# Kernel tuning notes

Measured on AMD Instinct MI355X. Metric: run time of the kernel, lower is better.

## Reference

```python
import jax, jax.numpy as jnp
import numpy as np

N, L, S, D = 8, 1024, 4096, 512
EPS = 1e-5

def layernorm(x, g, b):
    mu = jnp.mean(x, axis=-1, keepdims=True)
    var = jnp.var(x, axis=-1, keepdims=True)
    return (x - mu) * jax.lax.rsqrt(var + EPS) * g + b

def setup_inputs() -> dict:
    key = jax.random.key(0)
    ks = jax.random.split(key, 8)
    w = lambda k, shp: jax.random.normal(k, shp, dtype=jnp.float32) * 0.02
    return {
        "x": jax.random.normal(ks[0], (N, L, D), dtype=jnp.float32),
        "source": jax.random.normal(ks[1], (N, S, D), dtype=jnp.float32),
        "Wq": w(ks[2], (D, D)),
        "Wk": w(ks[3], (D, D)),
        "Wv": w(ks[4], (D, D)),
        "Wm": w(ks[5], (D, D)),
        "W1": w(ks[6], (2 * D, 2 * D)),
        "W2": w(ks[7], (2 * D, D)),
        "g1": jnp.ones((D,), jnp.float32),
        "b1": jnp.zeros((D,), jnp.float32),
        "g2": jnp.ones((D,), jnp.float32),
        "b2": jnp.zeros((D,), jnp.float32),
    }

def reference(x, source, Wq, Wk, Wv, Wm, W1, W2, g1, b1, g2, b2):
    # projections
    q = x @ Wq          # [N, L, D]
    k = source @ Wk     # [N, S, D]
    v = source @ Wv     # [N, S, D]
    # pairwise L2 distance via ||q||^2 + ||k||^2 - 2 q.k (avoids [N,L,S,D] tensor)
    q2 = jnp.sum(q * q, axis=-1)                      # [N, L]
    k2 = jnp.sum(k * k, axis=-1)                      # [N, S]
    qk = jnp.einsum('nlc,nsc->nls', q, k)             # [N, L, S]
    dist = jnp.sqrt(jnp.maximum(q2[:, :, None] + k2[:, None, :] - 2.0 * qk, 0.0))
    attn = jax.nn.softmax(dist, axis=2)               # softmax over S (note: +distance, as in source)
    message = jnp.einsum('nls,nsc->nlc', attn, v)     # [N, L, D]
    message = layernorm(message @ Wm, g1, b1)
    h = jnp.concatenate([x, message], axis=2)         # [N, L, 2D]
    message = jax.nn.relu(h @ W1) @ W2                # [N, L, D]
    message = layernorm(message, g2, b2)
    return x + message
```

## Files before the change

kernel.cpp:

```cpp
#include <hip/hip_runtime.h>
#include <stdint.h>

typedef unsigned short u16;
typedef __attribute__((ext_vector_type(8))) short bf16x8;
typedef __attribute__((ext_vector_type(4))) float f32x4;
typedef __attribute__((ext_vector_type(4))) unsigned int u32x4;

__device__ __forceinline__ u16 f2b(float f) {
  uint32_t u = __float_as_uint(f);
  u += 0x7fffu + ((u >> 16) & 1u);
  return (u16)(u >> 16);
}
__device__ __forceinline__ float b2f(u16 h) {
  return __uint_as_float(((uint32_t)h) << 16);
}
__device__ __forceinline__ uint32_t pack2bf(float a, float b) {
#if __has_builtin(__builtin_amdgcn_cvt_pk_bf16_f32)
  typedef __attribute__((ext_vector_type(2))) __bf16 bf16x2_t;
  bf16x2_t r = __builtin_amdgcn_cvt_pk_bf16_f32(a, b);
  return __builtin_bit_cast(uint32_t, r);
#else
  return (uint32_t)f2b(a) | ((uint32_t)f2b(b) << 16);
#endif
}
__device__ __forceinline__ float fast_sqrtf(float x) {
#if __has_builtin(__builtin_amdgcn_sqrtf)
  return __builtin_amdgcn_sqrtf(x);
#else
  return sqrtf(x);
#endif
}

__device__ __forceinline__ void gload_lds16(const u16* g, u16* l) {
  __builtin_amdgcn_global_load_lds(
      (const __attribute__((address_space(1))) void*)g,
      (__attribute__((address_space(3))) void*)l, 16, 0, 0);
}

enum { EPI_BF16_T = 0, EPI_BF16_T_SQ = 1, EPI_F32_T = 2, EPI_RELU_BF16_T = 3,
       EPI_EXP_T = 4 };

template <int EPI>
__device__ __forceinline__ void gemm_body(
    u16* smem, const u16* A, size_t sA, int lda,
    const u16* B, size_t sB, int ldb,
    void* C, size_t sC, int ldc, int K, size_t pStride,
    const float* e_col2, const float* e_row2, float* e_l,
    int lin, int gx, int gy) {
  u16* As = smem;
  u16* Bs = smem + 8192;
  const int t = threadIdx.x;
  const int batch = lin & 7;
  const int rest = lin >> 3;
  const int bx = rest % gx;
  const int ry = rest / gx;
  const int by = ry % gy;
  const int part = ry / gy;
  const int m0 = by * 128, n0 = bx * 128;
  const int koff = part * K;
  const u16* Ab = A + (size_t)batch * sA + (size_t)m0 * lda + koff;
  const u16* Bb = B + (size_t)batch * sB + (size_t)n0 * ldb + koff;
  const int srow = t >> 3;
  const int skey = (srow & 3) | (((srow >> 3) & 1) << 2);
  const int scol = ((t & 7) ^ skey) << 3;
  const u16* aS = Ab + (size_t)srow * lda + scol;
  const u16* bS = Bb + (size_t)srow * ldb + scol;
  const size_t a32 = (size_t)32 * lda, b32 = (size_t)32 * ldb;
  u16* asDst = As + t * 8;
  u16* bsDst = Bs + t * 8;

  const int w = t >> 6, lane = t & 63;
  const int wm = (w >> 1) << 6, wn = (w & 1) << 6;
  const int qd = lane >> 4, l16 = lane & 15;
  const int rbase = ((l16 >> 2) << 3) + (l16 & 3);
  const int keyA = (l16 & 3) | (((l16 >> 2) & 1) << 2);
  const int keyB = (l16 & 3) | (((l16 >> 3) & 1) << 2);
  const u16* aRow0 = As + (wm + rbase) * 64;
  const u16* bRow0 = Bs + (wn + l16) * 64;

  f32x4 acc[4][4];
#pragma unroll
  for (int i = 0; i < 4; i++)
#pragma unroll
    for (int j = 0; j < 4; j++) acc[i][j] = (f32x4)0.0f;

  for (int k0 = 0; k0 < K; k0 += 64) {
    gload_lds16(aS, asDst);
    gload_lds16(aS + a32, asDst + 2048);
    gload_lds16(aS + 2 * a32, asDst + 4096);
    gload_lds16(aS + 3 * a32, asDst + 6144);
    gload_lds16(bS, bsDst);
    gload_lds16(bS + b32, bsDst + 2048);
    gload_lds16(bS + 2 * b32, bsDst + 4096);
    gload_lds16(bS + 3 * b32, bsDst + 6144);
    aS += 64;
    bS += 64;
    __syncthreads();
#pragma unroll
    for (int s = 0; s < 2; s++) {
      const int ca = (((qd | (s << 2)) ^ keyA) << 3);
      const int cb = (((qd | (s << 2)) ^ keyB) << 3);
      bf16x8 af[4], bfr[4];
      af[0] = *(const bf16x8*)(aRow0 + ca);
      af[1] = *(const bf16x8*)(aRow0 + 4 * 64 + ca);
      af[2] = *(const bf16x8*)(aRow0 + 32 * 64 + ca);
      af[3] = *(const bf16x8*)(aRow0 + 36 * 64 + ca);
#pragma unroll
      for (int i = 0; i < 4; i++)
        bfr[i] = *(const bf16x8*)(bRow0 + i * 16 * 64 + cb);
#pragma unroll
      for (int mi = 0; mi < 4; mi++)
#pragma unroll
        for (int ni = 0; ni < 4; ni++)
          acc[mi][ni] = __builtin_amdgcn_mfma_f32_16x16x32_bf16(
              af[mi], bfr[ni], acc[mi][ni], 0, 0, 0);
    }
    __syncthreads();
  }

  const size_t cbase = (size_t)part * pStride + (size_t)batch * sC;
  const int ncols = (int)(sC / ldc);

  if constexpr (EPI == EPI_EXP_T) {
    const int nrows = (int)(sA / lda);
    const float* col2 = e_col2 + (size_t)batch * ncols;
    const float* row2 = e_row2 + (size_t)batch * nrows;
    float* lb = e_l + (size_t)batch * ncols;
    float c2v[4];
#pragma unroll
    for (int ni = 0; ni < 4; ni++) c2v[ni] = col2[n0 + wn + ni * 16 + l16];
    float cs[4] = {0.f, 0.f, 0.f, 0.f};
#pragma unroll
    for (int p = 0; p < 2; p++) {
      const int prow = m0 + wm + p * 32 + qd * 8;
      float r2v[8];
#pragma unroll
      for (int r8 = 0; r8 < 8; r8++) r2v[r8] = row2[prow + r8];
#pragma unroll
      for (int ni = 0; ni < 4; ni++) {
        const int col = n0 + wn + ni * 16 + l16;
        float pv[8];
#pragma unroll
        for (int r = 0; r < 4; r++) {
          pv[r] = __expf(fast_sqrtf(
              fmaxf(c2v[ni] + r2v[r] - 2.0f * acc[2 * p][ni][r], 0.0f)));
          pv[4 + r] = __expf(fast_sqrtf(
              fmaxf(c2v[ni] + r2v[4 + r] - 2.0f * acc[2 * p + 1][ni][r], 0.0f)));
        }
#pragma unroll
        for (int j = 0; j < 8; j++) cs[ni] += pv[j];
        u32x4 wv;
        wv[0] = pack2bf(pv[0], pv[1]);
        wv[1] = pack2bf(pv[2], pv[3]);
        wv[2] = pack2bf(pv[4], pv[5]);
        wv[3] = pack2bf(pv[6], pv[7]);
        *(u32x4*)((u16*)C + cbase + (size_t)col * ldc + prow) = wv;
      }
    }
#pragma unroll
    for (int ni = 0; ni < 4; ni++) {
      cs[ni] += __shfl_xor(cs[ni], 16);
      cs[ni] += __shfl_xor(cs[ni], 32);
    }
    if (qd == 0) {
#pragma unroll
      for (int ni = 0; ni < 4; ni++)
        atomicAdd(lb + n0 + wn + ni * 16 + l16, cs[ni]);
    }
  } else if constexpr (EPI == EPI_F32_T) {
#pragma unroll
    for (int p = 0; p < 2; p++) {
      const int prow = m0 + wm + p * 32 + qd * 8;
#pragma unroll
      for (int ni = 0; ni < 4; ni++) {
        const int col = n0 + wn + ni * 16 + l16;
        float* dst = (float*)C + cbase + (size_t)col * ldc + prow;
        *(f32x4*)dst = acc[2 * p][ni];
        *(f32x4*)(dst + 4) = acc[2 * p + 1][ni];
      }
    }
  } else {
    float cs[4] = {0.f, 0.f, 0.f, 0.f};
#pragma unroll
    for (int p = 0; p < 2; p++) {
      const int prow = m0 + wm + p * 32 + qd * 8;
#pragma unroll
      for (int ni = 0; ni < 4; ni++) {
        const int col = n0 + wn + ni * 16 + l16;
        float v[8];
#pragma unroll
        for (int r = 0; r < 4; r++) {
          v[r] = acc[2 * p][ni][r];
          v[4 + r] = acc[2 * p + 1][ni][r];
        }
        if (EPI == EPI_RELU_BF16_T) {
#pragma unroll
          for (int j = 0; j < 8; j++) v[j] = fmaxf(v[j], 0.0f);
        }
        if (EPI == EPI_BF16_T_SQ) {
#pragma unroll
          for (int j = 0; j < 8; j++) cs[ni] += v[j] * v[j];
        }
        u32x4 wv;
        wv[0] = pack2bf(v[0], v[1]);
        wv[1] = pack2bf(v[2], v[3]);
        wv[2] = pack2bf(v[4], v[5]);
        wv[3] = pack2bf(v[6], v[7]);
        *(u32x4*)((u16*)C + cbase + (size_t)col * ldc + prow) = wv;
      }
    }
    if (EPI == EPI_BF16_T_SQ) {
#pragma unroll
      for (int ni = 0; ni < 4; ni++) {
        cs[ni] += __shfl_xor(cs[ni], 16);
        cs[ni] += __shfl_xor(cs[ni], 32);
      }
      if (qd == 0) {
#pragma unroll
        for (int ni = 0; ni < 4; ni++)
          atomicAdd(e_l + (size_t)batch * ncols + n0 + wn + ni * 16 + l16,
                    cs[ni]);
      }
    }
  }
}

template <int EPI>
__global__ __launch_bounds__(256, 2) void gemm_nt(
    const u16* __restrict__ A, size_t sA, int lda,
    const u16* __restrict__ B, size_t sB, int ldb,
    void* __restrict__ C, size_t sC, int ldc, int K, size_t pStride,
    const float* __restrict__ e_col2, const float* __restrict__ e_row2,
    float* __restrict__ e_l) {
  __shared__ __align__(16) u16 smem[16384];
  const int lin = blockIdx.x + gridDim.x * (blockIdx.y + gridDim.y * blockIdx.z);
  gemm_body<EPI>(smem, A, sA, lda, B, sB, ldb, C, sC, ldc, K, pStride,
                 e_col2, e_row2, e_l, lin, gridDim.x, gridDim.y);
}

__global__ __launch_bounds__(256, 2) void proj_fused(
    const u16* __restrict__ WqT, const u16* __restrict__ WkT,
    const u16* __restrict__ WvT, const u16* __restrict__ h,
    const u16* __restrict__ sb, u16* __restrict__ q, u16* __restrict__ kb,
    u16* __restrict__ vT, float* __restrict__ q2, float* __restrict__ k2) {
  __shared__ __align__(16) u16 smem[16384];
  const int lin = blockIdx.x;
  if (lin < 256) {
    gemm_body<EPI_BF16_T_SQ>(smem, WqT, 0, 512, h, (size_t)1024 * 1024, 1024,
                             q, (size_t)1024 * 512, 512, 512, 0, nullptr,
                             nullptr, q2, lin, 8, 4);
  } else if (lin < 1280) {
    gemm_body<EPI_BF16_T_SQ>(smem, WkT, 0, 512, sb, (size_t)4096 * 512, 512,
                             kb, (size_t)4096 * 512, 512, 512, 0, nullptr,
                             nullptr, k2, lin - 256, 32, 4);
  } else {
    gemm_body<EPI_BF16_T>(smem, sb, (size_t)4096 * 512, 512, WvT, 0, 512,
                          vT, (size_t)512 * 4096, 4096, 512, 0, nullptr,
                          nullptr, nullptr, lin - 1280, 4, 32);
  }
}

__global__ __launch_bounds__(256) void reduce2_div_bf16(
    const float* __restrict__ P, const float* __restrict__ l,
    u16* __restrict__ out) {
  const size_t i = (size_t)blockIdx.x * 256 + threadIdx.x;
  const float4* p = (const float4*)P;
  float4 a = p[i];
  float4 b = p[i + 1048576];
  const float inv = 1.0f / l[i >> 7];
  ushort4 o = make_ushort4(f2b((a.x + b.x) * inv), f2b((a.y + b.y) * inv),
                           f2b((a.z + b.z) * inv), f2b((a.w + b.w) * inv));
  *(ushort4*)(out + (i << 2)) = o;
}

__global__ __launch_bounds__(256) void fused_prep(
    const float* __restrict__ x, const float* __restrict__ sc,
    u16* __restrict__ h, u16* __restrict__ sb, float* __restrict__ q2,
    float* __restrict__ k2, float* __restrict__ lsum) {
  const size_t i = (size_t)blockIdx.x * 256 + threadIdx.x;
  if (i < 1048576) {
    const float4 f = ((const float4*)x)[i];
    const int e = (int)(i << 2);
    const int row = e >> 9, col = e & 511;
    *(ushort4*)(h + ((size_t)row << 10) + col) =
        make_ushort4(f2b(f.x), f2b(f.y), f2b(f.z), f2b(f.w));
  } else if (i < 5242880) {
    const size_t j = i - 1048576;
    const float4 f = ((const float4*)sc)[j];
    *(ushort4*)(sb + (j << 2)) =
        make_ushort4(f2b(f.x), f2b(f.y), f2b(f.z), f2b(f.w));
  } else {
    const size_t j = i - 5242880;
    const float4 z = {0.f, 0.f, 0.f, 0.f};
    if (j < 2048) ((float4*)q2)[j] = z;
    else if (j < 10240) ((float4*)k2)[j - 2048] = z;
    else ((float4*)lsum)[j - 10240] = z;
  }
}

__global__ void transpose_w6(
    const float* __restrict__ Wq, const float* __restrict__ Wk,
    const float* __restrict__ Wv, const float* __restrict__ Wm,
    const float* __restrict__ W1, const float* __restrict__ W2,
    u16* __restrict__ WqT, u16* __restrict__ WkT, u16* __restrict__ WvT,
    u16* __restrict__ WmT, u16* __restrict__ W1T, u16* __restrict__ W2T) {
  __shared__ float tile[32][33];
  const float* W;
  u16* WT;
  int R, Cn;
  switch (blockIdx.z) {
    case 0: W = Wq; WT = WqT; R = 512; Cn = 512; break;
    case 1: W = Wk; WT = WkT; R = 512; Cn = 512; break;
    case 2: W = Wv; WT = WvT; R = 512; Cn = 512; break;
    case 3: W = Wm; WT = WmT; R = 512; Cn = 512; break;
    case 4: W = W1; WT = W1T; R = 1024; Cn = 1024; break;
    default: W = W2; WT = W2T; R = 1024; Cn = 512; break;
  }
  const int c0 = blockIdx.x * 32, r0 = blockIdx.y * 32;
  if (c0 >= Cn || r0 >= R) return;
  const int tx = threadIdx.x, ty = threadIdx.y;
  for (int i = ty; i < 32; i += 8) tile[i][tx] = W[(size_t)(r0 + i) * Cn + c0 + tx];
  __syncthreads();
  for (int i = ty; i < 32; i += 8) WT[(size_t)(c0 + i) * R + r0 + tx] = f2b(tile[tx][i]);
}

__global__ __launch_bounds__(128) void ln_to_h(const float* __restrict__ mm,
                                               const float* __restrict__ g,
                                               const float* __restrict__ b,
                                               u16* __restrict__ h) {
  const size_t row = blockIdx.x;
  const int t = threadIdx.x;
  const float4 fa = ((const float4*)(mm + row * 512))[t];
  const float4 fb = ((const float4*)(mm + 4194304 + row * 512))[t];
  float4 f;
  f.x = fa.x + fb.x; f.y = fa.y + fb.y; f.z = fa.z + fb.z; f.w = fa.w + fb.w;
  float s = f.x + f.y + f.z + f.w;
  float sq = f.x * f.x + f.y * f.y + f.z * f.z + f.w * f.w;
#pragma unroll
  for (int off = 32; off; off >>= 1) { s += __shfl_xor(s, off); sq += __shfl_xor(sq, off); }
  __shared__ float rs_[2], rq_[2];
  if ((t & 63) == 0) { rs_[t >> 6] = s; rq_[t >> 6] = sq; }
  __syncthreads();
  s = rs_[0] + rs_[1]; sq = rq_[0] + rq_[1];
  const float mu = s * (1.0f / 512.0f);
  const float rstd = rsqrtf(sq * (1.0f / 512.0f) - mu * mu + 1e-5f);
  const float4 gv = ((const float4*)g)[t], bv = ((const float4*)b)[t];
  ushort4 o = make_ushort4(f2b((f.x - mu) * rstd * gv.x + bv.x),
                           f2b((f.y - mu) * rstd * gv.y + bv.y),
                           f2b((f.z - mu) * rstd * gv.z + bv.z),
                           f2b((f.w - mu) * rstd * gv.w + bv.w));
  *(ushort4*)(h + (row << 10) + 512 + (t << 2)) = o;
}

__global__ __launch_bounds__(128) void ln_residual(const float* __restrict__ m2,
                                                   const float* __restrict__ x,
                                                   const float* __restrict__ g,
                                                   const float* __restrict__ b,
                                                   float* __restrict__ out) {
  const size_t row = blockIdx.x;
  const int t = threadIdx.x;
  const float4 fa = ((const float4*)(m2 + row * 512))[t];
  const float4 fb = ((const float4*)(m2 + 4194304 + row * 512))[t];
  float4 f;
  f.x = fa.x + fb.x; f.y = fa.y + fb.y; f.z = fa.z + fb.z; f.w = fa.w + fb.w;
  float s = f.x + f.y + f.z + f.w;
  float sq = f.x * f.x + f.y * f.y + f.z * f.z + f.w * f.w;
#pragma unroll
  for (int off = 32; off; off >>= 1) { s += __shfl_xor(s, off); sq += __shfl_xor(sq, off); }
  __shared__ float rs_[2], rq_[2];
  if ((t & 63) == 0) { rs_[t >> 6] = s; rq_[t >> 6] = sq; }
  __syncthreads();
  s = rs_[0] + rs_[1]; sq = rq_[0] + rq_[1];
  const float mu = s * (1.0f / 512.0f);
  const float rstd = rsqrtf(sq * (1.0f / 512.0f) - mu * mu + 1e-5f);
  const float4 gv = ((const float4*)g)[t], bv = ((const float4*)b)[t];
  const float4 xv = ((const float4*)(x + row * 512))[t];
  float4 o;
  o.x = xv.x + (f.x - mu) * rstd * gv.x + bv.x;
  o.y = xv.y + (f.y - mu) * rstd * gv.y + bv.y;
  o.z = xv.z + (f.z - mu) * rstd * gv.z + bv.z;
  o.w = xv.w + (f.w - mu) * rstd * gv.w + bv.w;
  ((float4*)(out + row * 512))[t] = o;
}

extern "C" void kernel_launch(void* const* d_in, const int* in_sizes, int n_in,
                              void* d_out, int out_size, void* d_ws, size_t ws_size,
                              hipStream_t stream) {
  const float* x  = (const float*)d_in[0];
  const float* sc = (const float*)d_in[1];
  const float* Wq = (const float*)d_in[2];
  const float* Wk = (const float*)d_in[3];
  const float* Wv = (const float*)d_in[4];
  const float* Wm = (const float*)d_in[5];
  const float* W1 = (const float*)d_in[6];
  const float* W2 = (const float*)d_in[7];
  const float* g1 = (const float*)d_in[8];
  const float* b1 = (const float*)d_in[9];
  const float* g2 = (const float*)d_in[10];
  const float* b2 = (const float*)d_in[11];
  float* out = (float*)d_out;
  char* ws = (char*)d_ws;

  constexpr int N = 8, L = 1024, S = 4096, D = 512;
  u16*   h   = (u16*)(ws + 0);
  u16*   sb  = (u16*)(ws + 16777216);
  u16*   WqT = (u16*)(ws + 50331648);
  u16*   WkT = (u16*)(ws + 50855936);
  u16*   WvT = (u16*)(ws + 51380224);
  u16*   WmT = (u16*)(ws + 51904512);
  u16*   W1T = (u16*)(ws + 52428800);
  u16*   W2T = (u16*)(ws + 54525952);
  u16*   q   = (u16*)(ws + 55574528);
  u16*   kb  = (u16*)(ws + 63963136);
  u16*   vT  = (u16*)(ws + 97517568);
  float* lsum= (float*)(ws + 131072000);
  float* q2  = (float*)(ws + 164626432);
  float* k2  = (float*)(ws + 164659200);
  u16*   qk  = (u16*)(ws + 164790272);
  u16*   msg = (u16*)(ws + 55574528);
  float* mpart = (float*)(ws + 63963136);
  float* mm  = (float*)(ws + 63963136);
  u16*   hh  = (u16*)(ws + 80740352);
  float* m2  = (float*)(ws + 97517568);

  fused_prep<<<dim3(20528), 256, 0, stream>>>(x, sc, h, sb, q2, k2, lsum);
  transpose_w6<<<dim3(32, 32, 6), dim3(32, 8), 0, stream>>>(
      Wq, Wk, Wv, Wm, W1, W2, WqT, WkT, WvT, WmT, W1T, W2T);

  proj_fused<<<dim3(2304), 256, 0, stream>>>(WqT, WkT, WvT, h, sb, q, kb, vT,
                                             q2, k2);

  gemm_nt<EPI_EXP_T><<<dim3(8, 32, 8), 256, 0, stream>>>(
      kb, (size_t)S * 512, 512, q, (size_t)L * 512, 512, qk, (size_t)L * S, S,
      512, 0, q2, k2, lsum);
  gemm_nt<EPI_F32_T><<<dim3(8, 4, 16), 256, 0, stream>>>(
      vT, (size_t)D * S, S, qk, (size_t)L * S, S, mpart, (size_t)L * 512, 512,
      2048, (size_t)(N * L) * 512, nullptr, nullptr, nullptr);
  reduce2_div_bf16<<<dim3(4096), 256, 0, stream>>>(mpart, lsum, msg);

  gemm_nt<EPI_F32_T><<<dim3(8, 4, 16), 256, 0, stream>>>(
      WmT, 0, 512, msg, (size_t)L * 512, 512, mm, (size_t)L * 512, 512, 256,
      (size_t)(N * L) * 512, nullptr, nullptr, nullptr);
  ln_to_h<<<dim3(N * L), 128, 0, stream>>>(mm, g1, b1, h);

  gemm_nt<EPI_RELU_BF16_T><<<dim3(8, 8, 8), 256, 0, stream>>>(
      W1T, 0, 1024, h, (size_t)L * 1024, 1024, hh, (size_t)L * 1024, 1024, 1024,
      0, nullptr, nullptr, nullptr);
  gemm_nt<EPI_F32_T><<<dim3(8, 4, 16), 256, 0, stream>>>(
      W2T, 0, 1024, hh, (size_t)L * 1024, 1024, m2, (size_t)L * 512, 512, 512,
      (size_t)(N * L) * 512, nullptr, nullptr, nullptr);

  ln_residual<<<dim3(N * L), 128, 0, stream>>>(m2, x, g2, b2, out);
}
```

Baseline: 355.3 us.

## Merge prep kernels, fold split-K reduce into Wm GEMM via duplicated weights

Merges the input conversion and weight transpose launches into one prep kernel. The split-K attention-times-V partials are now written as bf16 side by side (row width 1024). The Wm projection consumes them against a horizontally duplicated WmT, so the K-sum happens inside that GEMM and the 1/lsum normalization moves into ln_to_h. This removes the reduce2_div kernel and its fp32 partial round-trip. It also swaps the block index order for the q/k projections. The risk is that rounding the unnormalized partials to bf16 changes precision, and the Wm GEMM now runs a K of 1024 instead of 512.

```diff
diff --git a/kernel.cpp b/kernel.cpp
--- a/kernel.cpp
+++ b/kernel.cpp
@@ -40,7 +40,7 @@
 enum { EPI_BF16_T = 0, EPI_BF16_T_SQ = 1, EPI_F32_T = 2, EPI_RELU_BF16_T = 3,
        EPI_EXP_T = 4 };
 
-template <int EPI>
+template <int EPI, bool BYFAST = false>
 __device__ __forceinline__ void gemm_body(
     u16* smem, const u16* A, size_t sA, int lda,
     const u16* B, size_t sB, int ldb,
@@ -52,10 +52,18 @@
   const int t = threadIdx.x;
   const int batch = lin & 7;
   const int rest = lin >> 3;
-  const int bx = rest % gx;
-  const int ry = rest / gx;
-  const int by = ry % gy;
-  const int part = ry / gy;
+  int bx, by, part;
+  if (BYFAST) {
+    by = rest % gy;
+    const int rx = rest / gy;
+    bx = rx % gx;
+    part = rx / gx;
+  } else {
+    bx = rest % gx;
+    const int ry = rest / gx;
+    by = ry % gy;
+    part = ry / gy;
+  }
   const int m0 = by * 128, n0 = bx * 128;
   const int koff = part * K;
   const u16* Ab = A + (size_t)batch * sA + (size_t)m0 * lda + koff;
@@ -246,13 +254,13 @@
   __shared__ __align__(16) u16 smem[16384];
   const int lin = blockIdx.x;
   if (lin < 256) {
-    gemm_body<EPI_BF16_T_SQ>(smem, WqT, 0, 512, h, (size_t)1024 * 1024, 1024,
-                             q, (size_t)1024 * 512, 512, 512, 0, nullptr,
-                             nullptr, q2, lin, 8, 4);
+    gemm_body<EPI_BF16_T_SQ, true>(smem, WqT, 0, 512, h, (size_t)1024 * 1024,
+                                   1024, q, (size_t)1024 * 512, 512, 512, 0,
+                                   nullptr, nullptr, q2, lin, 8, 4);
   } else if (lin < 1280) {
-    gemm_body<EPI_BF16_T_SQ>(smem, WkT, 0, 512, sb, (size_t)4096 * 512, 512,
-                             kb, (size_t)4096 * 512, 512, 512, 0, nullptr,
-                             nullptr, k2, lin - 256, 32, 4);
+    gemm_body<EPI_BF16_T_SQ, true>(smem, WkT, 0, 512, sb, (size_t)4096 * 512,
+                                   512, kb, (size_t)4096 * 512, 512, 512, 0,
+                                   nullptr, nullptr, k2, lin - 256, 32, 4);
   } else {
     gemm_body<EPI_BF16_T>(smem, sb, (size_t)4096 * 512, 512, WvT, 0, 512,
                           vT, (size_t)512 * 4096, 4096, 512, 0, nullptr,
@@ -260,80 +268,86 @@
   }
 }
 
-__global__ __launch_bounds__(256) void reduce2_div_bf16(
-    const float* __restrict__ P, const float* __restrict__ l,
-    u16* __restrict__ out) {
-  const size_t i = (size_t)blockIdx.x * 256 + threadIdx.x;
-  const float4* p = (const float4*)P;
-  float4 a = p[i];
-  float4 b = p[i + 1048576];
-  const float inv = 1.0f / l[i >> 7];
-  ushort4 o = make_ushort4(f2b((a.x + b.x) * inv), f2b((a.y + b.y) * inv),
-                           f2b((a.z + b.z) * inv), f2b((a.w + b.w) * inv));
-  *(ushort4*)(out + (i << 2)) = o;
-}
-
-__global__ __launch_bounds__(256) void fused_prep(
+__global__ __launch_bounds__(256) void prep_all(
     const float* __restrict__ x, const float* __restrict__ sc,
     u16* __restrict__ h, u16* __restrict__ sb, float* __restrict__ q2,
-    float* __restrict__ k2, float* __restrict__ lsum) {
-  const size_t i = (size_t)blockIdx.x * 256 + threadIdx.x;
-  if (i < 1048576) {
-    const float4 f = ((const float4*)x)[i];
-    const int e = (int)(i << 2);
-    const int row = e >> 9, col = e & 511;
-    *(ushort4*)(h + ((size_t)row << 10) + col) =
-        make_ushort4(f2b(f.x), f2b(f.y), f2b(f.z), f2b(f.w));
-  } else if (i < 5242880) {
-    const size_t j = i - 1048576;
-    const float4 f = ((const float4*)sc)[j];
-    *(ushort4*)(sb + (j << 2)) =
-        make_ushort4(f2b(f.x), f2b(f.y), f2b(f.z), f2b(f.w));
-  } else {
-    const size_t j = i - 5242880;
-    const float4 z = {0.f, 0.f, 0.f, 0.f};
-    if (j < 2048) ((float4*)q2)[j] = z;
-    else if (j < 10240) ((float4*)k2)[j - 2048] = z;
-    else ((float4*)lsum)[j - 10240] = z;
-  }
-}
-
-__global__ void transpose_w6(
+    float* __restrict__ k2, float* __restrict__ lsum,
     const float* __restrict__ Wq, const float* __restrict__ Wk,
     const float* __restrict__ Wv, const float* __restrict__ Wm,
     const float* __restrict__ W1, const float* __restrict__ W2,
     u16* __restrict__ WqT, u16* __restrict__ WkT, u16* __restrict__ WvT,
-    u16* __restrict__ WmT, u16* __restrict__ W1T, u16* __restrict__ W2T) {
+    u16* __restrict__ WmT2, u16* __restrict__ W1T, u16* __restrict__ W2T) {
   __shared__ float tile[32][33];
+  const int blk = blockIdx.x;
+  if (blk < 20528) {
+    const size_t i = (size_t)blk * 256 + threadIdx.x;
+    if (i < 1048576) {
+      const float4 f = ((const float4*)x)[i];
+      const int e = (int)(i << 2);
+      const int row = e >> 9, col = e & 511;
+      *(ushort4*)(h + ((size_t)row << 10) + col) =
+          make_ushort4(f2b(f.x), f2b(f.y), f2b(f.z), f2b(f.w));
+    } else if (i < 5242880) {
+      const size_t j = i - 1048576;
+      const float4 f = ((const float4*)sc)[j];
+      *(ushort4*)(sb + (j << 2)) =
+          make_ushort4(f2b(f.x), f2b(f.y), f2b(f.z), f2b(f.w));
+    } else {
+      const size_t j = i - 5242880;
+      const float4 z = {0.f, 0.f, 0.f, 0.f};
+      if (j < 2048) ((float4*)q2)[j] = z;
+      else if (j < 10240) ((float4*)k2)[j - 2048] = z;
+      else ((float4*)lsum)[j - 10240] = z;
+    }
+    return;
+  }
+  const int tb = blk - 20528;
   const float* W;
   u16* WT;
-  int R, Cn;
-  switch (blockIdx.z) {
-    case 0: W = Wq; WT = WqT; R = 512; Cn = 512; break;
-    case 1: W = Wk; WT = WkT; R = 512; Cn = 512; break;
-    case 2: W = Wv; WT = WvT; R = 512; Cn = 512; break;
-    case 3: W = Wm; WT = WmT; R = 512; Cn = 512; break;
-    case 4: W = W1; WT = W1T; R = 1024; Cn = 1024; break;
-    default: W = W2; WT = W2T; R = 1024; Cn = 512; break;
-  }
-  const int c0 = blockIdx.x * 32, r0 = blockIdx.y * 32;
-  if (c0 >= Cn || r0 >= R) return;
-  const int tx = threadIdx.x, ty = threadIdx.y;
-  for (int i = ty; i < 32; i += 8) tile[i][tx] = W[(size_t)(r0 + i) * Cn + c0 + tx];
+  int R, Cn, ldT, dup = 0, c0, r0;
+  if (tb < 1024) {
+    const int z = tb >> 8, local = tb & 255;
+    switch (z) {
+      case 0: W = Wq; WT = WqT; break;
+      case 1: W = Wk; WT = WkT; break;
+      case 2: W = Wv; WT = WvT; break;
+      default: W = Wm; WT = WmT2; dup = 1; break;
+    }
+    R = 512; Cn = 512; ldT = dup ? 1024 : 512;
+    c0 = (local & 15) << 5; r0 = (local >> 4) << 5;
+  } else if (tb < 2048) {
+    const int local = tb - 1024;
+    W = W1; WT = W1T; R = 1024; Cn = 1024; ldT = 1024;
+    c0 = (local & 31) << 5; r0 = (local >> 5) << 5;
+  } else {
+    const int local = tb - 2048;
+    W = W2; WT = W2T; R = 1024; Cn = 512; ldT = 1024;
+    c0 = (local & 15) << 5; r0 = (local >> 4) << 5;
+  }
+  const int tx = threadIdx.x & 31, ty = threadIdx.x >> 5;
+  for (int i = ty; i < 32; i += 8)
+    tile[i][tx] = W[(size_t)(r0 + i) * Cn + c0 + tx];
   __syncthreads();
-  for (int i = ty; i < 32; i += 8) WT[(size_t)(c0 + i) * R + r0 + tx] = f2b(tile[tx][i]);
+  for (int i = ty; i < 32; i += 8) {
+    const u16 v = f2b(tile[tx][i]);
+    WT[(size_t)(c0 + i) * ldT + r0 + tx] = v;
+    if (dup) WT[(size_t)(c0 + i) * ldT + 512 + r0 + tx] = v;
+  }
 }
 
 __global__ __launch_bounds__(128) void ln_to_h(const float* __restrict__ mm,
+                                               const float* __restrict__ lsum,
                                                const float* __restrict__ g,
                                                const float* __restrict__ b,
                                                u16* __restrict__ h) {
   const size_t row = blockIdx.x;
   const int t = threadIdx.x;
+  const float inv = 1.0f / lsum[row];
   const float4 fa = ((const float4*)(mm + row * 512))[t];
   const float4 fb = ((const float4*)(mm + 4194304 + row * 512))[t];
   float4 f;
-  f.x = fa.x + fb.x; f.y = fa.y + fb.y; f.z = fa.z + fb.z; f.w = fa.w + fb.w;
+  f.x = (fa.x + fb.x) * inv; f.y = (fa.y + fb.y) * inv;
+  f.z = (fa.z + fb.z) * inv; f.w = (fa.w + fb.w) * inv;
   float s = f.x + f.y + f.z + f.w;
   float sq = f.x * f.x + f.y * f.y + f.z * f.z + f.w * f.w;
 #pragma unroll
@@ -402,30 +416,29 @@
   char* ws = (char*)d_ws;
 
   constexpr int N = 8, L = 1024, S = 4096, D = 512;
-  u16*   h   = (u16*)(ws + 0);
-  u16*   sb  = (u16*)(ws + 16777216);
-  u16*   WqT = (u16*)(ws + 50331648);
-  u16*   WkT = (u16*)(ws + 50855936);
-  u16*   WvT = (u16*)(ws + 51380224);
-  u16*   WmT = (u16*)(ws + 51904512);
-  u16*   W1T = (u16*)(ws + 52428800);
-  u16*   W2T = (u16*)(ws + 54525952);
-  u16*   q   = (u16*)(ws + 55574528);
-  u16*   kb  = (u16*)(ws + 63963136);
-  u16*   vT  = (u16*)(ws + 97517568);
-  float* lsum= (float*)(ws + 131072000);
-  float* q2  = (float*)(ws + 164626432);
-  float* k2  = (float*)(ws + 164659200);
-  u16*   qk  = (u16*)(ws + 164790272);
-  u16*   msg = (u16*)(ws + 55574528);
-  float* mpart = (float*)(ws + 63963136);
-  float* mm  = (float*)(ws + 63963136);
-  u16*   hh  = (u16*)(ws + 80740352);
-  float* m2  = (float*)(ws + 97517568);
-
-  fused_prep<<<dim3(20528), 256, 0, stream>>>(x, sc, h, sb, q2, k2, lsum);
-  transpose_w6<<<dim3(32, 32, 6), dim3(32, 8), 0, stream>>>(
-      Wq, Wk, Wv, Wm, W1, W2, WqT, WkT, WvT, WmT, W1T, W2T);
+  u16*   h    = (u16*)(ws + 0);
+  u16*   sb   = (u16*)(ws + 16777216);
+  u16*   WqT  = (u16*)(ws + 50331648);
+  u16*   WkT  = (u16*)(ws + 50855936);
+  u16*   WvT  = (u16*)(ws + 51380224);
+  u16*   WmT2 = (u16*)(ws + 51904512);
+  u16*   W1T  = (u16*)(ws + 52953088);
+  u16*   W2T  = (u16*)(ws + 55050240);
+  u16*   q    = (u16*)(ws + 56098816);
+  u16*   kb   = (u16*)(ws + 64487424);
+  u16*   vT   = (u16*)(ws + 98041856);
+  float* lsum = (float*)(ws + 131596288);
+  float* q2   = (float*)(ws + 131629056);
+  float* k2   = (float*)(ws + 131661824);
+  u16*   qk   = (u16*)(ws + 164790272);
+  u16*   msg2 = (u16*)(ws + 56098816);
+  float* mm   = (float*)(ws + 72876032);
+  u16*   hh   = (u16*)(ws + 72876032);
+  float* m2   = (float*)(ws + 98041856);
+
+  prep_all<<<dim3(23088), 256, 0, stream>>>(x, sc, h, sb, q2, k2, lsum,
+                                            Wq, Wk, Wv, Wm, W1, W2,
+                                            WqT, WkT, WvT, WmT2, W1T, W2T);
 
   proj_fused<<<dim3(2304), 256, 0, stream>>>(WqT, WkT, WvT, h, sb, q, kb, vT,
                                              q2, k2);
@@ -433,15 +446,14 @@
   gemm_nt<EPI_EXP_T><<<dim3(8, 32, 8), 256, 0, stream>>>(
       kb, (size_t)S * 512, 512, q, (size_t)L * 512, 512, qk, (size_t)L * S, S,
       512, 0, q2, k2, lsum);
+  gemm_nt<EPI_BF16_T><<<dim3(8, 4, 16), 256, 0, stream>>>(
+      vT, (size_t)D * S, S, qk, (size_t)L * S, S, msg2, (size_t)L * 1024, 1024,
+      2048, 512, nullptr, nullptr, nullptr);
+
   gemm_nt<EPI_F32_T><<<dim3(8, 4, 16), 256, 0, stream>>>(
-      vT, (size_t)D * S, S, qk, (size_t)L * S, S, mpart, (size_t)L * 512, 512,
-      2048, (size_t)(N * L) * 512, nullptr, nullptr, nullptr);
-  reduce2_div_bf16<<<dim3(4096), 256, 0, stream>>>(mpart, lsum, msg);
-
-  gemm_nt<EPI_F32_T><<<dim3(8, 4, 16), 256, 0, stream>>>(
-      WmT, 0, 512, msg, (size_t)L * 512, 512, mm, (size_t)L * 512, 512, 256,
-      (size_t)(N * L) * 512, nullptr, nullptr, nullptr);
-  ln_to_h<<<dim3(N * L), 128, 0, stream>>>(mm, g1, b1, h);
+      WmT2, 0, 1024, msg2, (size_t)L * 1024, 1024, mm, (size_t)L * 512, 512,
+      512, (size_t)(N * L) * 512, nullptr, nullptr, nullptr);
+  ln_to_h<<<dim3(N * L), 128, 0, stream>>>(mm, lsum, g1, b1, h);
 
   gemm_nt<EPI_RELU_BF16_T><<<dim3(8, 8, 8), 256, 0, stream>>>(
       W1T, 0, 1024, h, (size_t)L * 1024, 1024, hh, (size_t)L * 1024, 1024, 1024,
```

Result: no change. 352.9 us (-0.6%).
